# Performance work log

Hardware: AMD Instinct MI355X
Metric: run time of the kernel (lower is better)

The kernel has to match this reference:

```python
import jax, jax.numpy as jnp
import numpy as np

D = 128            # actual_dim / embed_dim
DM = 2 * D         # d_model
HID = 2 * DM       # LSTMCell hidden size
NSYM = 200000
PAD = NSYM
B = 4096
S = 5
NB = 64
STEPS = 4
EPS = 1e-6


def setup_inputs() -> dict:
    key = jax.random.key(0)
    ks = jax.random.split(key, 24)
    def rn(k, sh, scale=0.02):
        return jax.random.normal(k, sh, dtype=jnp.float32) * scale
    emb = rn(ks[10], (NSYM + 1, D)).at[PAD].set(0.0)  # padding row zeroed
    inp = {
        'query': jax.random.randint(ks[0], (B, 2), 0, NSYM),
        'support': jax.random.randint(ks[1], (S, 2), 0, NSYM),
        'q_l_conn': jax.random.randint(ks[2], (B, NB, 2), 0, NSYM),
        'q_l_deg': jax.random.randint(ks[3], (B,), 0, NB),
        'q_r_conn': jax.random.randint(ks[4], (B, NB, 2), 0, NSYM),
        'q_r_deg': jax.random.randint(ks[5], (B,), 0, NB),
        's_l_conn': jax.random.randint(ks[6], (S, NB, 2), 0, NSYM),
        's_l_deg': jax.random.randint(ks[7], (S,), 0, NB),
        's_r_conn': jax.random.randint(ks[8], (S, NB, 2), 0, NSYM),
        's_r_deg': jax.random.randint(ks[9], (S,), 0, NB),
        'emb': emb,
        'gcn_w': rn(ks[11], (D, 2 * D)),
        'gcn_bias': jnp.zeros((D,), jnp.float32),
        'proj1_w': rn(ks[12], (2 * DM, DM)),
        'proj1_b': jnp.zeros((2 * DM,), jnp.float32),
        'proj2_w': rn(ks[13], (DM, 2 * DM)),
        'proj2_b': jnp.zeros((DM,), jnp.float32),
        'ln_g': jnp.ones((DM,), jnp.float32),
        'ln_b': jnp.zeros((DM,), jnp.float32),
        'w_ih': rn(ks[14], (4 * HID, DM)),
        'w_hh': rn(ks[15], (4 * HID, HID)),
        'b_ih': jnp.zeros((4 * HID,), jnp.float32),
        'b_hh': jnp.zeros((4 * HID,), jnp.float32),
    }
    return inp


def _neighbor_encoder(conn, deg, emb, gcn_w, gcn_bias):
    # conn: [N, NB, 2] ids (rel, ent); deg: [N]
    rel = emb[conn[:, :, 0]]                     # [N, NB, D] gather
    ent = emb[conn[:, :, 1]]                     # [N, NB, D] gather
    x = jnp.concatenate([rel, ent], axis=-1)     # [N, NB, 2D]
    out = jnp.einsum('bnd,kd->bnk', x, gcn_w) + gcn_bias  # [N, NB, D]
    denom = jnp.maximum(deg, 1).astype(out.dtype)[:, None]
    return jnp.tanh(out.sum(axis=1) / denom)     # [N, D]


def _support_encoder(x, proj1_w, proj1_b, proj2_w, proj2_b, ln_g, ln_b):
    residual = x
    h = jax.nn.relu(x @ proj1_w.T + proj1_b)
    h = h @ proj2_w.T + proj2_b
    z = h + residual
    mu = z.mean(axis=-1, keepdims=True)
    sigma = jnp.std(z, axis=-1, keepdims=True, ddof=1)
    return ln_g * (z - mu) / (sigma + EPS) + ln_b


def _query_encoder(support_vec, query, w_ih, w_hh, b_ih, b_hh):
    # support_vec: [DM] (single support prototype); query: [B, DM]
    bsz = query.shape[0]
    h_r = jnp.zeros((bsz, HID), query.dtype)
    c = jnp.zeros((bsz, HID), query.dtype)
    xW = query @ w_ih.T + b_ih  # invariant across steps
    h = query
    for _ in range(STEPS):
        gates = xW + h_r @ w_hh.T + b_hh
        i, f, g, o = jnp.split(gates, 4, axis=-1)
        c = jax.nn.sigmoid(f) * c + jax.nn.sigmoid(i) * jnp.tanh(g)
        h_cell = jax.nn.sigmoid(o) * jnp.tanh(c)
        h = query + h_cell[:, :DM]
        # attention over a single support row: softmax of one logit == 1
        r = jnp.broadcast_to(support_vec[None, :], h.shape)
        h_r = jnp.concatenate([h, r], axis=-1)
    return h


def reference(query, support, q_l_conn, q_l_deg, q_r_conn, q_r_deg,
              s_l_conn, s_l_deg, s_r_conn, s_r_deg,
              emb, gcn_w, gcn_bias, proj1_w, proj1_b, proj2_w, proj2_b,
              ln_g, ln_b, w_ih, w_hh, b_ih, b_hh):
    ql = _neighbor_encoder(q_l_conn, q_l_deg, emb, gcn_w, gcn_bias)
    qr = _neighbor_encoder(q_r_conn, q_r_deg, emb, gcn_w, gcn_bias)
    sl = _neighbor_encoder(s_l_conn, s_l_deg, emb, gcn_w, gcn_bias)
    sr = _neighbor_encoder(s_r_conn, s_r_deg, emb, gcn_w, gcn_bias)
    query_nb = jnp.concatenate([ql, qr], axis=-1)    # [B, DM]
    support_nb = jnp.concatenate([sl, sr], axis=-1)  # [S, DM]
    se = lambda x: _support_encoder(x, proj1_w, proj1_b, proj2_w, proj2_b, ln_g, ln_b)
    support_g = se(support_nb).mean(axis=0)          # [DM]
    query_g = se(query_nb)                            # [B, DM]
    query_f = _query_encoder(support_g, query_g, w_ih, w_hh, b_ih, b_hh)
    qn = query_f / jnp.maximum(jnp.linalg.norm(query_f, axis=-1, keepdims=True), 1e-12)
    sn = support_g / jnp.maximum(jnp.linalg.norm(support_g), 1e-12)
    return qn @ sn                                    # [B] matching scores
```

## Files before the change

### kernel.cpp

```cpp
#include <hip/hip_runtime.h>

#define BQ 4096
#define NS 5

typedef __attribute__((ext_vector_type(8))) short bf16x8;
typedef __attribute__((ext_vector_type(4))) float f32x4;
typedef unsigned short ushortT;

#define WS_QNB    0
#define WS_Z      1048576
#define WS_QG     2097152
#define WS_XW     3145728
#define WS_CBUF   5242880
#define WS_XS     6291456
#define WS_H1B    7348224
#define WS_ABF    7872512
#define WS_HB1    8134656
#define WS_P1B    8396800
#define WS_P2B    8462336
#define WS_WIHB   8527872
#define WS_WHHB   8658944
#define WS_GWB    8790016
#define WS_SNB    8806400
#define WS_H1G    8807680
#define WS_ZB     8810240
#define WS_SG     8811520
#define WS_SN     8811776
#define WS_SWL    8812032
#define WS_BL     8813056
#define WS_EMB16  8814080
#define EMB_ELEMS 25600128

__device__ __forceinline__ float wave_allreduce(float v) {
#pragma unroll
  for (int off = 32; off > 0; off >>= 1) v += __shfl_xor(v, off, 64);
  return v;
}
__device__ __forceinline__ float block_allreduce(float v, float* buf) {
  v = wave_allreduce(v);
  __syncthreads();
  if ((threadIdx.x & 63) == 0) buf[threadIdx.x >> 6] = v;
  __syncthreads();
  return buf[0] + buf[1] + buf[2] + buf[3];
}
__device__ __forceinline__ float sigm(float x) { return 1.0f / (1.0f + expf(-x)); }
__device__ __forceinline__ ushortT f2bf(float f) {
  unsigned int u = __float_as_uint(f);
  unsigned int r = (u + 0x7fffu + ((u >> 16) & 1u)) >> 16;
  return (ushortT)r;
}
__device__ __forceinline__ float bf2f(ushortT u) {
  return __uint_as_float(((unsigned int)u) << 16);
}
__device__ __forceinline__ float dot4(float4 a, float4 b) {
  return a.x * b.x + a.y * b.y + a.z * b.z + a.w * b.w;
}

__global__ __launch_bounds__(256) void k_prep(
    const float* __restrict__ emb, ushortT* __restrict__ emb16, int doEmb,
    const float* __restrict__ w_ih, const float* __restrict__ w_hh,
    const float* __restrict__ p1w, const float* __restrict__ p2w,
    const float* __restrict__ gcn_w,
    const float* __restrict__ b_ih, const float* __restrict__ b_hh,
    ushortT* __restrict__ p1b16, ushortT* __restrict__ p2b16,
    ushortT* __restrict__ wihb, ushortT* __restrict__ whhb,
    ushortT* __restrict__ gwb, float* __restrict__ bL) {
  const int gid = blockIdx.x * 256 + threadIdx.x;
  const int stride = gridDim.x * 256;
  if (doEmb) {
    const float4* e4 = (const float4*)emb;
    ushort4* o4 = (ushort4*)emb16;
    for (int i = gid; i < EMB_ELEMS / 4; i += stride) {
      float4 v = e4[i];
      ushort4 u;
      u.x = f2bf(v.x); u.y = f2bf(v.y); u.z = f2bf(v.z); u.w = f2bf(v.w);
      o4[i] = u;
    }
  }
  for (int i = gid; i < 131072; i += stride) p1b16[i] = f2bf(p1w[i]);
  for (int i = gid; i < 131072; i += stride) p2b16[i] = f2bf(p2w[i]);
  for (int i = gid; i < 262144; i += stride) {
    int n = i >> 8, k = i & 255;
    int j = (n >> 2) + 512 * (n & 3);
    wihb[i] = f2bf(w_ih[j * 256 + k]);
    whhb[i] = f2bf(w_hh[j * 512 + k]);
  }
  for (int i = gid; i < 32768; i += stride) gwb[i] = f2bf(gcn_w[i]);
  for (int i = gid; i < 1024; i += stride) {
    int j = (i >> 2) + 512 * (i & 3);
    bL[i] = b_ih[j] + b_hh[j];
  }
}

__global__ __launch_bounds__(256) void k_gather16(
    const int* __restrict__ qlc, const int* __restrict__ qrc,
    const int* __restrict__ slc, const int* __restrict__ src_,
    const ushortT* __restrict__ emb16, ushortT* __restrict__ XS) {
  const int r = blockIdx.x;
  const int b = r >> 1, side = r & 1;
  const int t = threadIdx.x;
  const int* cg;
  if (b < BQ) cg = (side ? qrc : qlc) + (size_t)b * 128;
  else        cg = (side ? src_ : slc) + (size_t)(b - BQ) * 128;
  __shared__ int connS[128];
  __shared__ __align__(16) float part[8][132];
  if (t < 128) connS[t] = cg[t];
  __syncthreads();
  const int s = t >> 5, l = t & 31;
  const ushort4* e2 = (const ushort4*)emb16;
  float4 acc = make_float4(0.f, 0.f, 0.f, 0.f);
  int im[16];
#pragma unroll
  for (int k = 0; k < 16; k++) im[k] = connS[k * 8 + s];
  ushort4 v[16];
#pragma unroll
  for (int k = 0; k < 16; k++) v[k] = e2[(size_t)im[k] * 32 + l];
#pragma unroll
  for (int k = 0; k < 16; k++) {
    acc.x += bf2f(v[k].x); acc.y += bf2f(v[k].y);
    acc.z += bf2f(v[k].z); acc.w += bf2f(v[k].w);
  }
  *(float4*)&part[s][l * 4] = acc;
  __syncthreads();
  const int hf = t >> 7, dd = t & 127;
  float sum = part[hf][dd] + part[2 + hf][dd] + part[4 + hf][dd] + part[6 + hf][dd];
  XS[(size_t)r * 256 + t] = f2bf(sum);
}

__global__ __launch_bounds__(256) void k_gather32(
    const int* __restrict__ qlc, const int* __restrict__ qrc,
    const int* __restrict__ slc, const int* __restrict__ src_,
    const float* __restrict__ emb, ushortT* __restrict__ XS) {
  const int r = blockIdx.x;
  const int b = r >> 1, side = r & 1;
  const int t = threadIdx.x;
  const int* cg;
  if (b < BQ) cg = (side ? qrc : qlc) + (size_t)b * 128;
  else        cg = (side ? src_ : slc) + (size_t)(b - BQ) * 128;
  __shared__ int connS[128];
  __shared__ __align__(16) float part[8][132];
  if (t < 128) connS[t] = cg[t];
  __syncthreads();
  const int s = t >> 5, l = t & 31;
  const float4* emb4 = (const float4*)emb;
  float4 acc = make_float4(0.f, 0.f, 0.f, 0.f);
#pragma unroll
  for (int kb = 0; kb < 2; kb++) {
    int im[8];
#pragma unroll
    for (int k = 0; k < 8; k++) im[k] = connS[(kb * 8 + k) * 8 + s];
    float4 v[8];
#pragma unroll
    for (int k = 0; k < 8; k++) v[k] = emb4[(size_t)im[k] * 32 + l];
#pragma unroll
    for (int k = 0; k < 8; k++) {
      acc.x += v[k].x; acc.y += v[k].y; acc.z += v[k].z; acc.w += v[k].w;
    }
  }
  *(float4*)&part[s][l * 4] = acc;
  __syncthreads();
  const int hf = t >> 7, dd = t & 127;
  float sum = part[hf][dd] + part[2 + hf][dd] + part[4 + hf][dd] + part[6 + hf][dd];
  XS[(size_t)r * 256 + t] = f2bf(sum);
}

__global__ __launch_bounds__(256) void k_gcn(
    const ushortT* __restrict__ XS, const ushortT* __restrict__ gwb,
    const float* __restrict__ gcn_bias,
    const int* __restrict__ qld, const int* __restrict__ qrd,
    const int* __restrict__ sld, const int* __restrict__ srd,
    float* __restrict__ qnb, float* __restrict__ snb, ushortT* __restrict__ xq) {
  __shared__ short As[64 * 40];
  __shared__ short Bs[128 * 40];
  __shared__ int degl[32], degr[32];
  const int t = threadIdx.x;
  const int row0 = blockIdx.x * 64;
  if (t < 32) {
    int b = (row0 >> 1) + t;
    int dl = 1, dr = 1;
    if (b < BQ) { dl = qld[b]; dr = qrd[b]; }
    else if (b < BQ + NS) { dl = sld[b - BQ]; dr = srd[b - BQ]; }
    degl[t] = (dl > 0) ? dl : 1;
    degr[t] = (dr > 0) ? dr : 1;
  }
  const int wave = t >> 6, lane = t & 63;
  const int wm = wave >> 1, wn = wave & 1, quad = lane >> 4, mr = lane & 15;
  f32x4 acc[2][4];
#pragma unroll
  for (int mi = 0; mi < 2; mi++)
#pragma unroll
    for (int ni = 0; ni < 4; ni++) acc[mi][ni] = (f32x4){0.f, 0.f, 0.f, 0.f};
  const int arow = t >> 2, akc = t & 3;
  for (int k0 = 0; k0 < 256; k0 += 32) {
    float4 av = *(const float4*)(XS + (size_t)(row0 + arow) * 256 + k0 + akc * 8);
    float4 bv0 = *(const float4*)(gwb + (size_t)arow * 256 + k0 + akc * 8);
    float4 bv1 = *(const float4*)(gwb + (size_t)(64 + arow) * 256 + k0 + akc * 8);
    __syncthreads();
    *(float4*)&As[arow * 40 + akc * 8] = av;
    *(float4*)&Bs[arow * 40 + akc * 8] = bv0;
    *(float4*)&Bs[(64 + arow) * 40 + akc * 8] = bv1;
    __syncthreads();
    bf16x8 af[2], bfr[4];
#pragma unroll
    for (int mi = 0; mi < 2; mi++)
      af[mi] = *(const bf16x8*)&As[(wm * 32 + mi * 16 + mr) * 40 + quad * 8];
#pragma unroll
    for (int ni = 0; ni < 4; ni++)
      bfr[ni] = *(const bf16x8*)&Bs[(wn * 64 + ni * 16 + mr) * 40 + quad * 8];
#pragma unroll
    for (int mi = 0; mi < 2; mi++)
#pragma unroll
      for (int ni = 0; ni < 4; ni++)
        acc[mi][ni] = __builtin_amdgcn_mfma_f32_16x16x32_bf16(af[mi], bfr[ni], acc[mi][ni], 0, 0, 0);
  }
#pragma unroll
  for (int mi = 0; mi < 2; mi++) {
#pragma unroll
    for (int ni = 0; ni < 4; ni++) {
      const int col = wn * 64 + ni * 16 + mr;
      const int rb = row0 + wm * 32 + mi * 16 + quad * 4;
      const float bs = 64.0f * gcn_bias[col];
#pragma unroll
      for (int reg = 0; reg < 4; reg++) {
        const int row = rb + reg;
        const int b = row >> 1, side = row & 1;
        if (b >= BQ + NS) continue;
        const int li = (row >> 1) - (row0 >> 1);
        const int deg = side ? degr[li] : degl[li];
        float val = tanhf((acc[mi][ni][reg] + bs) / (float)deg);
        if (b < BQ) {
          const size_t o = (size_t)b * 256 + side * 128 + col;
          qnb[o] = val;
          xq[o] = f2bf(val);
        } else {
          snb[(size_t)(b - BQ) * 256 + side * 128 + col] = val;
        }
      }
    }
  }
}

__global__ __launch_bounds__(256) void k_proj1(
    const ushortT* __restrict__ A, const ushortT* __restrict__ B,
    const float* __restrict__ bias, ushortT* __restrict__ outb,
    const float* __restrict__ snb, const float* __restrict__ p1w,
    const float* __restrict__ p1b, float* __restrict__ h1g) {
  __shared__ short As[64 * 40];
  __shared__ short Bs[128 * 40];
  const int t = threadIdx.x;
  if (blockIdx.x >= 256) {
    const int w = (blockIdx.x - 256) * 4 + (t >> 6);
    const int lane = t & 63;
    const int r = w >> 9, j = w & 511;
    float4 x = *(const float4*)&snb[r * 256 + lane * 4];
    float4 wv = *(const float4*)&p1w[(size_t)j * 256 + lane * 4];
    float s = wave_allreduce(dot4(x, wv));
    if (lane == 0) h1g[r * 512 + j] = fmaxf(s + p1b[j], 0.f);
    return;
  }
  const int bn = blockIdx.x % 4, bm = blockIdx.x / 4;
  const int row0 = bm * 64, col0 = bn * 128;
  const int wave = t >> 6, lane = t & 63;
  const int wm = wave >> 1, wn = wave & 1, quad = lane >> 4, mr = lane & 15;
  f32x4 acc[2][4];
#pragma unroll
  for (int mi = 0; mi < 2; mi++)
#pragma unroll
    for (int ni = 0; ni < 4; ni++) acc[mi][ni] = (f32x4){0.f, 0.f, 0.f, 0.f};
  const int arow = t >> 2, akc = t & 3;
  for (int k0 = 0; k0 < 256; k0 += 32) {
    float4 av = *(const float4*)(A + (size_t)(row0 + arow) * 256 + k0 + akc * 8);
    float4 bv0 = *(const float4*)(B + (size_t)(col0 + arow) * 256 + k0 + akc * 8);
    float4 bv1 = *(const float4*)(B + (size_t)(col0 + 64 + arow) * 256 + k0 + akc * 8);
    __syncthreads();
    *(float4*)&As[arow * 40 + akc * 8] = av;
    *(float4*)&Bs[arow * 40 + akc * 8] = bv0;
    *(float4*)&Bs[(64 + arow) * 40 + akc * 8] = bv1;
    __syncthreads();
    bf16x8 af[2], bfr[4];
#pragma unroll
    for (int mi = 0; mi < 2; mi++)
      af[mi] = *(const bf16x8*)&As[(wm * 32 + mi * 16 + mr) * 40 + quad * 8];
#pragma unroll
    for (int ni = 0; ni < 4; ni++)
      bfr[ni] = *(const bf16x8*)&Bs[(wn * 64 + ni * 16 + mr) * 40 + quad * 8];
#pragma unroll
    for (int mi = 0; mi < 2; mi++)
#pragma unroll
      for (int ni = 0; ni < 4; ni++)
        acc[mi][ni] = __builtin_amdgcn_mfma_f32_16x16x32_bf16(af[mi], bfr[ni], acc[mi][ni], 0, 0, 0);
  }
#pragma unroll
  for (int mi = 0; mi < 2; mi++) {
#pragma unroll
    for (int ni = 0; ni < 4; ni++) {
      const int col = col0 + wn * 64 + ni * 16 + mr;
      const int rb = row0 + wm * 32 + mi * 16 + quad * 4;
      const float bs = bias[col];
#pragma unroll
      for (int reg = 0; reg < 4; reg++) {
        const int row = rb + reg;
        outb[(size_t)row * 512 + col] = f2bf(fmaxf(acc[mi][ni][reg] + bs, 0.f));
      }
    }
  }
}

__global__ __launch_bounds__(256) void k_proj2(
    const ushortT* __restrict__ A, const ushortT* __restrict__ B,
    const float* __restrict__ bias, const float* __restrict__ aux,
    float* __restrict__ outf,
    const float* __restrict__ snb, const float* __restrict__ h1g,
    const float* __restrict__ p2w, const float* __restrict__ p2b,
    float* __restrict__ zb) {
  __shared__ short As[64 * 40];
  __shared__ short Bs[128 * 40];
  const int t = threadIdx.x;
  if (blockIdx.x >= 128) {
    const int w = (blockIdx.x - 128) * 4 + (t >> 6);
    const int lane = t & 63;
    const int r = w >> 8, tt = w & 255;
    float4 h0 = *(const float4*)&h1g[r * 512 + lane * 4];
    float4 h1 = *(const float4*)&h1g[r * 512 + 256 + lane * 4];
    float4 w0 = *(const float4*)&p2w[(size_t)tt * 512 + lane * 4];
    float4 w1 = *(const float4*)&p2w[(size_t)tt * 512 + 256 + lane * 4];
    float s = wave_allreduce(dot4(h0, w0) + dot4(h1, w1));
    if (lane == 0) zb[r * 256 + tt] = s + p2b[tt] + snb[r * 256 + tt];
    return;
  }
  const int bn = blockIdx.x % 2, bm = blockIdx.x / 2;
  const int row0 = bm * 64, col0 = bn * 128;
  const int wave = t >> 6, lane = t & 63;
  const int wm = wave >> 1, wn = wave & 1, quad = lane >> 4, mr = lane & 15;
  f32x4 acc[2][4];
#pragma unroll
  for (int mi = 0; mi < 2; mi++)
#pragma unroll
    for (int ni = 0; ni < 4; ni++) acc[mi][ni] = (f32x4){0.f, 0.f, 0.f, 0.f};
  const int arow = t >> 2, akc = t & 3;
  for (int k0 = 0; k0 < 512; k0 += 32) {
    float4 av = *(const float4*)(A + (size_t)(row0 + arow) * 512 + k0 + akc * 8);
    float4 bv0 = *(const float4*)(B + (size_t)(col0 + arow) * 512 + k0 + akc * 8);
    float4 bv1 = *(const float4*)(B + (size_t)(col0 + 64 + arow) * 512 + k0 + akc * 8);
    __syncthreads();
    *(float4*)&As[arow * 40 + akc * 8] = av;
    *(float4*)&Bs[arow * 40 + akc * 8] = bv0;
    *(float4*)&Bs[(64 + arow) * 40 + akc * 8] = bv1;
    __syncthreads();
    bf16x8 af[2], bfr[4];
#pragma unroll
    for (int mi = 0; mi < 2; mi++)
      af[mi] = *(const bf16x8*)&As[(wm * 32 + mi * 16 + mr) * 40 + quad * 8];
#pragma unroll
    for (int ni = 0; ni < 4; ni++)
      bfr[ni] = *(const bf16x8*)&Bs[(wn * 64 + ni * 16 + mr) * 40 + quad * 8];
#pragma unroll
    for (int mi = 0; mi < 2; mi++)
#pragma unroll
      for (int ni = 0; ni < 4; ni++)
        acc[mi][ni] = __builtin_amdgcn_mfma_f32_16x16x32_bf16(af[mi], bfr[ni], acc[mi][ni], 0, 0, 0);
  }
#pragma unroll
  for (int mi = 0; mi < 2; mi++) {
#pragma unroll
    for (int ni = 0; ni < 4; ni++) {
      const int col = col0 + wn * 64 + ni * 16 + mr;
      const int rb = row0 + wm * 32 + mi * 16 + quad * 4;
      const float bs = bias[col];
#pragma unroll
      for (int reg = 0; reg < 4; reg++) {
        const int row = rb + reg;
        const size_t off = (size_t)row * 256 + col;
        outf[off] = acc[mi][ni][reg] + bs + aux[off];
      }
    }
  }
}

__global__ __launch_bounds__(256) void k_ln2(
    const float* __restrict__ Z, const float* __restrict__ ln_g,
    const float* __restrict__ ln_b, float* __restrict__ qg, ushortT* __restrict__ qgb,
    const float* __restrict__ zb, float* __restrict__ sg, float* __restrict__ sn_out) {
  const int t = threadIdx.x;
  if (blockIdx.x >= BQ / 4) {
    __shared__ float rbuf[4];
    float acc = 0.f;
    for (int r = 0; r < NS; r++) {
      float z = zb[r * 256 + t];
      float s = block_allreduce(z, rbuf);
      float mu = s * (1.f / 256.f);
      float dz = z - mu;
      float s2 = block_allreduce(dz * dz, rbuf);
      float rstd = 1.f / (sqrtf(s2 * (1.f / 255.f)) + 1e-6f);
      acc += ln_g[t] * dz * rstd + ln_b[t];
      __syncthreads();
    }
    float g = acc * (1.f / (float)NS);
    sg[t] = g;
    float n2 = block_allreduce(g * g, rbuf);
    sn_out[t] = g / fmaxf(sqrtf(n2), 1e-12f);
    return;
  }
  const int row = blockIdx.x * 4 + (t >> 6);
  const int lane = t & 63;
  float4 z = *(const float4*)&Z[(size_t)row * 256 + lane * 4];
  float s = wave_allreduce(z.x + z.y + z.z + z.w);
  float mu = s * (1.f / 256.f);
  float dx = z.x - mu, dy = z.y - mu, dz = z.z - mu, dw = z.w - mu;
  float s2 = wave_allreduce(dx * dx + dy * dy + dz * dz + dw * dw);
  float rstd = 1.f / (sqrtf(s2 * (1.f / 255.f)) + 1e-6f);
  float4 g = *(const float4*)&ln_g[lane * 4];
  float4 bb = *(const float4*)&ln_b[lane * 4];
  float4 o;
  o.x = g.x * dx * rstd + bb.x;
  o.y = g.y * dy * rstd + bb.y;
  o.z = g.z * dz * rstd + bb.z;
  o.w = g.w * dw * rstd + bb.w;
  *(float4*)&qg[(size_t)row * 256 + lane * 4] = o;
  ushort4 u;
  u.x = f2bf(o.x); u.y = f2bf(o.y); u.z = f2bf(o.z); u.w = f2bf(o.w);
  *(ushort4*)&qgb[(size_t)row * 256 + lane * 4] = u;
}

__global__ __launch_bounds__(256) void k_gemm_lstm(
    const ushortT* __restrict__ A, const ushortT* __restrict__ B,
    const float* __restrict__ bL, float* __restrict__ sWl,
    const float* __restrict__ qg, ushortT* __restrict__ xwb,
    float* __restrict__ cbuf, ushortT* __restrict__ hb_out,
    const float* __restrict__ sg, const float* __restrict__ w_hh, int phase) {
  __shared__ short As[64 * 40];
  __shared__ short Bs[128 * 40];
  __shared__ __align__(16) float Cs[64 * 132];
  const int t = threadIdx.x;
  if (blockIdx.x >= 512) {
    const int n = (blockIdx.x - 512) * 4 + (t >> 6);
    const int lane = t & 63;
    const int j = (n >> 2) + 512 * (n & 3);
    float4 x = *(const float4*)&sg[lane * 4];
    float4 wv = *(const float4*)&w_hh[(size_t)j * 512 + 256 + lane * 4];
    float s = wave_allreduce(dot4(x, wv));
    if (lane == 0) sWl[n] = s;
    return;
  }
  const int bn = blockIdx.x & 7, bm = blockIdx.x >> 3;
  const int row0 = bm * 64, col0 = bn * 128;
  const int wave = t >> 6, lane = t & 63;
  const int wm = wave >> 1, wn = wave & 1, quad = lane >> 4, mr = lane & 15;
  f32x4 acc[2][4];
#pragma unroll
  for (int mi = 0; mi < 2; mi++)
#pragma unroll
    for (int ni = 0; ni < 4; ni++) acc[mi][ni] = (f32x4){0.f, 0.f, 0.f, 0.f};
  const int arow = t >> 2, akc = t & 3;
  for (int k0 = 0; k0 < 256; k0 += 32) {
    float4 av = *(const float4*)(A + (size_t)(row0 + arow) * 256 + k0 + akc * 8);
    float4 bv0 = *(const float4*)(B + (size_t)(col0 + arow) * 256 + k0 + akc * 8);
    float4 bv1 = *(const float4*)(B + (size_t)(col0 + 64 + arow) * 256 + k0 + akc * 8);
    __syncthreads();
    *(float4*)&As[arow * 40 + akc * 8] = av;
    *(float4*)&Bs[arow * 40 + akc * 8] = bv0;
    *(float4*)&Bs[(64 + arow) * 40 + akc * 8] = bv1;
    __syncthreads();
    bf16x8 af[2], bfr[4];
#pragma unroll
    for (int mi = 0; mi < 2; mi++)
      af[mi] = *(const bf16x8*)&As[(wm * 32 + mi * 16 + mr) * 40 + quad * 8];
#pragma unroll
    for (int ni = 0; ni < 4; ni++)
      bfr[ni] = *(const bf16x8*)&Bs[(wn * 64 + ni * 16 + mr) * 40 + quad * 8];
#pragma unroll
    for (int mi = 0; mi < 2; mi++)
#pragma unroll
      for (int ni = 0; ni < 4; ni++)
        acc[mi][ni] = __builtin_amdgcn_mfma_f32_16x16x32_bf16(af[mi], bfr[ni], acc[mi][ni], 0, 0, 0);
  }
#pragma unroll
  for (int mi = 0; mi < 2; mi++)
#pragma unroll
    for (int ni = 0; ni < 4; ni++)
#pragma unroll
      for (int reg = 0; reg < 4; reg++)
        Cs[(wm * 32 + mi * 16 + quad * 4 + reg) * 132 + wn * 64 + ni * 16 + mr] =
            acc[mi][ni][reg];
  __syncthreads();
  const int u = t & 31, grp = t >> 5;
  const int ugl = bn * 32 + u;
#pragma unroll
  for (int i = 0; i < 8; i++) {
    const int rl = grp * 8 + i;
    const int row = row0 + rl;
    const size_t o = (size_t)row * 256 + ugl;
    float4 gv = *(const float4*)&Cs[rl * 132 + u * 4];
    if (phase == 0) {
      float4 bb = *(const float4*)&bL[col0 + u * 4];
      gv.x += bb.x; gv.y += bb.y; gv.z += bb.z; gv.w += bb.w;
      float c0 = sigm(gv.x) * tanhf(gv.z);
      float h = qg[o] + sigm(gv.w) * tanhf(c0);
      cbuf[o] = c0;
      hb_out[o] = f2bf(h);
      ushort4 xo;
      xo.x = f2bf(gv.x); xo.y = f2bf(gv.y);
      xo.z = f2bf(gv.z); xo.w = f2bf(gv.w);
      *(ushort4*)&xwb[(size_t)row * 1024 + col0 + u * 4] = xo;
    } else {
      ushort4 xv = *(const ushort4*)&xwb[(size_t)row * 1024 + col0 + u * 4];
      float4 sv = *(const float4*)&sWl[col0 + u * 4];
      gv.x += bf2f(xv.x) + sv.x; gv.y += bf2f(xv.y) + sv.y;
      gv.z += bf2f(xv.z) + sv.z; gv.w += bf2f(xv.w) + sv.w;
      float c = sigm(gv.y) * cbuf[o] + sigm(gv.x) * tanhf(gv.z);
      float h = qg[o] + sigm(gv.w) * tanhf(c);
      if (phase == 2) {
        cbuf[o] = h;
      } else {
        cbuf[o] = c;
        hb_out[o] = f2bf(h);
      }
    }
  }
}

__global__ __launch_bounds__(256) void k_out(
    const float* __restrict__ hf, const float* __restrict__ sn, float* __restrict__ out) {
  const int t = threadIdx.x;
  const int row = blockIdx.x * 4 + (t >> 6);
  const int lane = t & 63;
  float4 h = *(const float4*)&hf[(size_t)row * 256 + lane * 4];
  float4 s = *(const float4*)&sn[lane * 4];
  float dt = wave_allreduce(dot4(h, s));
  float nr = wave_allreduce(dot4(h, h));
  if (lane == 0) out[row] = dt / fmaxf(sqrtf(nr), 1e-12f);
}

extern "C" void kernel_launch(void* const* d_in, const int* in_sizes, int n_in,
                              void* d_out, int out_size, void* d_ws, size_t ws_size,
                              hipStream_t stream) {
  const int* q_l_conn = (const int*)d_in[2];
  const int* q_l_deg  = (const int*)d_in[3];
  const int* q_r_conn = (const int*)d_in[4];
  const int* q_r_deg  = (const int*)d_in[5];
  const int* s_l_conn = (const int*)d_in[6];
  const int* s_l_deg  = (const int*)d_in[7];
  const int* s_r_conn = (const int*)d_in[8];
  const int* s_r_deg  = (const int*)d_in[9];
  const float* emb      = (const float*)d_in[10];
  const float* gcn_w    = (const float*)d_in[11];
  const float* gcn_bias = (const float*)d_in[12];
  const float* proj1_w  = (const float*)d_in[13];
  const float* proj1_b  = (const float*)d_in[14];
  const float* proj2_w  = (const float*)d_in[15];
  const float* proj2_b  = (const float*)d_in[16];
  const float* ln_g     = (const float*)d_in[17];
  const float* ln_b     = (const float*)d_in[18];
  const float* w_ih     = (const float*)d_in[19];
  const float* w_hh     = (const float*)d_in[20];
  const float* b_ih     = (const float*)d_in[21];
  const float* b_hh     = (const float*)d_in[22];

  float* ws = (float*)d_ws;
  float* qnb   = ws + WS_QNB;
  float* Z     = ws + WS_Z;
  float* qg    = ws + WS_QG;
  ushortT* xwb = (ushortT*)(ws + WS_XW);
  float* cbuf  = ws + WS_CBUF;
  ushortT* XS    = (ushortT*)(ws + WS_XS);
  ushortT* h1b   = (ushortT*)(ws + WS_H1B);
  ushortT* abf   = (ushortT*)(ws + WS_ABF);
  ushortT* hb1   = (ushortT*)(ws + WS_HB1);
  ushortT* p1b16 = (ushortT*)(ws + WS_P1B);
  ushortT* p2b16 = (ushortT*)(ws + WS_P2B);
  ushortT* wihb  = (ushortT*)(ws + WS_WIHB);
  ushortT* whhb  = (ushortT*)(ws + WS_WHHB);
  ushortT* gwb   = (ushortT*)(ws + WS_GWB);
  float* snb   = ws + WS_SNB;
  float* h1g   = ws + WS_H1G;
  float* zb    = ws + WS_ZB;
  float* sg    = ws + WS_SG;
  float* sn    = ws + WS_SN;
  float* sWl   = ws + WS_SWL;
  float* bL    = ws + WS_BL;
  ushortT* emb16 = (ushortT*)(ws + WS_EMB16);
  float* out   = (float*)d_out;

  const size_t needF = (size_t)WS_EMB16 + (EMB_ELEMS + 1) / 2;
  const int useBf16 = (ws_size >= needF * sizeof(float)) ? 1 : 0;

  hipLaunchKernelGGL(k_prep, dim3(2048), dim3(256), 0, stream,
                     emb, emb16, useBf16,
                     w_ih, w_hh, proj1_w, proj2_w, gcn_w, b_ih, b_hh,
                     p1b16, p2b16, wihb, whhb, gwb, bL);
  if (useBf16) {
    hipLaunchKernelGGL(k_gather16, dim3(2 * (BQ + NS)), dim3(256), 0, stream,
                       q_l_conn, q_r_conn, s_l_conn, s_r_conn, emb16, XS);
  } else {
    hipLaunchKernelGGL(k_gather32, dim3(2 * (BQ + NS)), dim3(256), 0, stream,
                       q_l_conn, q_r_conn, s_l_conn, s_r_conn, emb, XS);
  }
  hipLaunchKernelGGL(k_gcn, dim3(129), dim3(256), 0, stream,
                     XS, gwb, gcn_bias, q_l_deg, q_r_deg, s_l_deg, s_r_deg,
                     qnb, snb, abf);
  hipLaunchKernelGGL(k_proj1, dim3(256 + 640), dim3(256), 0, stream,
                     abf, p1b16, proj1_b, h1b,
                     snb, proj1_w, proj1_b, h1g);
  hipLaunchKernelGGL(k_proj2, dim3(128 + 320), dim3(256), 0, stream,
                     h1b, p2b16, proj2_b, qnb, Z,
                     snb, h1g, proj2_w, proj2_b, zb);
  hipLaunchKernelGGL(k_ln2, dim3(BQ / 4 + 1), dim3(256), 0, stream,
                     Z, ln_g, ln_b, qg, abf, zb, sg, sn);
  hipLaunchKernelGGL(k_gemm_lstm, dim3(512 + 256), dim3(256), 0, stream,
                     abf, wihb, bL, sWl, qg, xwb, cbuf, hb1, sg, w_hh, 0);
  hipLaunchKernelGGL(k_gemm_lstm, dim3(512), dim3(256), 0, stream,
                     hb1, whhb, bL, sWl, qg, xwb, cbuf, abf, sg, w_hh, 1);
  hipLaunchKernelGGL(k_gemm_lstm, dim3(512), dim3(256), 0, stream,
                     abf, whhb, bL, sWl, qg, xwb, cbuf, hb1, sg, w_hh, 1);
  hipLaunchKernelGGL(k_gemm_lstm, dim3(512), dim3(256), 0, stream,
                     hb1, whhb, bL, sWl, qg, xwb, cbuf, (ushortT*)nullptr, sg, w_hh, 2);
  hipLaunchKernelGGL(k_out, dim3(BQ / 4), dim3(256), 0, stream, cbuf, sn, out);
}
```

Measured before the change: 333.1 us.

## Fuse all four LSTM steps and the output dot into one row-strip kernel

Replaces the four separate LSTM GEMM launches and the output kernel with a single kernel in which each block owns 16 query rows and runs every step, keeping h, c and the query state in shared memory. The constant support half of the hidden input is now folded into the GEMM as a K=512 bf16 weight (with a bf16 copy of support_g) instead of a separate fp32 matvec. This removes the global round-trips of xw, c and h between steps and several launches. In exchange it launches only 256 blocks, each streaming the whole weight matrix from global/L2 without LDS staging, and adds K work for the support part.

```diff
diff --git a/kernel.cpp b/kernel.cpp
--- a/kernel.cpp
+++ b/kernel.cpp
@@ -10,7 +10,7 @@
 #define WS_QNB    0
 #define WS_Z      1048576
 #define WS_QG     2097152
-#define WS_XW     3145728
+#define WS_WHH2   3145728
 #define WS_CBUF   5242880
 #define WS_XS     6291456
 #define WS_H1B    7348224
@@ -26,7 +26,7 @@
 #define WS_ZB     8810240
 #define WS_SG     8811520
 #define WS_SN     8811776
-#define WS_SWL    8812032
+#define WS_SGB    8812032
 #define WS_BL     8813056
 #define WS_EMB16  8814080
 #define EMB_ELEMS 25600128
@@ -63,7 +63,7 @@
     const float* __restrict__ gcn_w,
     const float* __restrict__ b_ih, const float* __restrict__ b_hh,
     ushortT* __restrict__ p1b16, ushortT* __restrict__ p2b16,
-    ushortT* __restrict__ wihb, ushortT* __restrict__ whhb,
+    ushortT* __restrict__ wihb, ushortT* __restrict__ whh2,
     ushortT* __restrict__ gwb, float* __restrict__ bL) {
   const int gid = blockIdx.x * 256 + threadIdx.x;
   const int stride = gridDim.x * 256;
@@ -83,7 +83,11 @@
     int n = i >> 8, k = i & 255;
     int j = (n >> 2) + 512 * (n & 3);
     wihb[i] = f2bf(w_ih[j * 256 + k]);
-    whhb[i] = f2bf(w_hh[j * 512 + k]);
+  }
+  for (int i = gid; i < 524288; i += stride) {
+    int n = i >> 9, k = i & 511;
+    int j = (n >> 2) + 512 * (n & 3);
+    whh2[i] = f2bf(w_hh[j * 512 + k]);
   }
   for (int i = gid; i < 32768; i += stride) gwb[i] = f2bf(gcn_w[i]);
   for (int i = gid; i < 1024; i += stride) {
@@ -99,12 +103,12 @@
   const int r = blockIdx.x;
   const int b = r >> 1, side = r & 1;
   const int t = threadIdx.x;
-  const int* cg;
-  if (b < BQ) cg = (side ? qrc : qlc) + (size_t)b * 128;
-  else        cg = (side ? src_ : slc) + (size_t)(b - BQ) * 128;
+  const int* cg2;
+  if (b < BQ) cg2 = (side ? qrc : qlc) + (size_t)b * 128;
+  else        cg2 = (side ? src_ : slc) + (size_t)(b - BQ) * 128;
   __shared__ int connS[128];
   __shared__ __align__(16) float part[8][132];
-  if (t < 128) connS[t] = cg[t];
+  if (t < 128) connS[t] = cg2[t];
   __syncthreads();
   const int s = t >> 5, l = t & 31;
   const ushort4* e2 = (const ushort4*)emb16;
@@ -134,12 +138,12 @@
   const int r = blockIdx.x;
   const int b = r >> 1, side = r & 1;
   const int t = threadIdx.x;
-  const int* cg;
-  if (b < BQ) cg = (side ? qrc : qlc) + (size_t)b * 128;
-  else        cg = (side ? src_ : slc) + (size_t)(b - BQ) * 128;
+  const int* cg2;
+  if (b < BQ) cg2 = (side ? qrc : qlc) + (size_t)b * 128;
+  else        cg2 = (side ? src_ : slc) + (size_t)(b - BQ) * 128;
   __shared__ int connS[128];
   __shared__ __align__(16) float part[8][132];
-  if (t < 128) connS[t] = cg[t];
+  if (t < 128) connS[t] = cg2[t];
   __syncthreads();
   const int s = t >> 5, l = t & 31;
   const float4* emb4 = (const float4*)emb;
@@ -380,7 +384,8 @@
 __global__ __launch_bounds__(256) void k_ln2(
     const float* __restrict__ Z, const float* __restrict__ ln_g,
     const float* __restrict__ ln_b, float* __restrict__ qg, ushortT* __restrict__ qgb,
-    const float* __restrict__ zb, float* __restrict__ sg, float* __restrict__ sn_out) {
+    const float* __restrict__ zb, float* __restrict__ sg, float* __restrict__ sn_out,
+    ushortT* __restrict__ sgb) {
   const int t = threadIdx.x;
   if (blockIdx.x >= BQ / 4) {
     __shared__ float rbuf[4];
@@ -397,6 +402,7 @@
     }
     float g = acc * (1.f / (float)NS);
     sg[t] = g;
+    sgb[t] = f2bf(g);
     float n2 = block_allreduce(g * g, rbuf);
     sn_out[t] = g / fmaxf(sqrtf(n2), 1e-12f);
     return;
@@ -422,113 +428,100 @@
   *(ushort4*)&qgb[(size_t)row * 256 + lane * 4] = u;
 }
 
-__global__ __launch_bounds__(256) void k_gemm_lstm(
-    const ushortT* __restrict__ A, const ushortT* __restrict__ B,
-    const float* __restrict__ bL, float* __restrict__ sWl,
-    const float* __restrict__ qg, ushortT* __restrict__ xwb,
-    float* __restrict__ cbuf, ushortT* __restrict__ hb_out,
-    const float* __restrict__ sg, const float* __restrict__ w_hh, int phase) {
-  __shared__ short As[64 * 40];
-  __shared__ short Bs[128 * 40];
-  __shared__ __align__(16) float Cs[64 * 132];
+__global__ __launch_bounds__(256) void k_lstm_strip(
+    const ushortT* __restrict__ qgb, const float* __restrict__ qg,
+    const ushortT* __restrict__ wihb, const ushortT* __restrict__ whh2,
+    const float* __restrict__ bL, const ushortT* __restrict__ sgb,
+    const float* __restrict__ sn, float* __restrict__ out) {
+  __shared__ __align__(16) ushortT hS[16][264];
+  __shared__ __align__(16) float qgS[16][256];
+  __shared__ __align__(16) float cS[16][256];
+  __shared__ __align__(16) float hF[16][256];
+  __shared__ __align__(16) ushortT sgS[264];
   const int t = threadIdx.x;
-  if (blockIdx.x >= 512) {
-    const int n = (blockIdx.x - 512) * 4 + (t >> 6);
-    const int lane = t & 63;
-    const int j = (n >> 2) + 512 * (n & 3);
-    float4 x = *(const float4*)&sg[lane * 4];
-    float4 wv = *(const float4*)&w_hh[(size_t)j * 512 + 256 + lane * 4];
-    float s = wave_allreduce(dot4(x, wv));
-    if (lane == 0) sWl[n] = s;
-    return;
-  }
-  const int bn = blockIdx.x & 7, bm = blockIdx.x >> 3;
-  const int row0 = bm * 64, col0 = bn * 128;
-  const int wave = t >> 6, lane = t & 63;
-  const int wm = wave >> 1, wn = wave & 1, quad = lane >> 4, mr = lane & 15;
-  f32x4 acc[2][4];
-#pragma unroll
-  for (int mi = 0; mi < 2; mi++)
-#pragma unroll
-    for (int ni = 0; ni < 4; ni++) acc[mi][ni] = (f32x4){0.f, 0.f, 0.f, 0.f};
-  const int arow = t >> 2, akc = t & 3;
-  for (int k0 = 0; k0 < 256; k0 += 32) {
-    float4 av = *(const float4*)(A + (size_t)(row0 + arow) * 256 + k0 + akc * 8);
-    float4 bv0 = *(const float4*)(B + (size_t)(col0 + arow) * 256 + k0 + akc * 8);
-    float4 bv1 = *(const float4*)(B + (size_t)(col0 + 64 + arow) * 256 + k0 + akc * 8);
-    __syncthreads();
-    *(float4*)&As[arow * 40 + akc * 8] = av;
-    *(float4*)&Bs[arow * 40 + akc * 8] = bv0;
-    *(float4*)&Bs[(64 + arow) * 40 + akc * 8] = bv1;
-    __syncthreads();
-    bf16x8 af[2], bfr[4];
-#pragma unroll
-    for (int mi = 0; mi < 2; mi++)
-      af[mi] = *(const bf16x8*)&As[(wm * 32 + mi * 16 + mr) * 40 + quad * 8];
-#pragma unroll
-    for (int ni = 0; ni < 4; ni++)
-      bfr[ni] = *(const bf16x8*)&Bs[(wn * 64 + ni * 16 + mr) * 40 + quad * 8];
-#pragma unroll
-    for (int mi = 0; mi < 2; mi++)
-#pragma unroll
-      for (int ni = 0; ni < 4; ni++)
-        acc[mi][ni] = __builtin_amdgcn_mfma_f32_16x16x32_bf16(af[mi], bfr[ni], acc[mi][ni], 0, 0, 0);
-  }
-#pragma unroll
-  for (int mi = 0; mi < 2; mi++)
-#pragma unroll
-    for (int ni = 0; ni < 4; ni++)
-#pragma unroll
-      for (int reg = 0; reg < 4; reg++)
-        Cs[(wm * 32 + mi * 16 + quad * 4 + reg) * 132 + wn * 64 + ni * 16 + mr] =
-            acc[mi][ni][reg];
+  const int w = t >> 6, lane = t & 63;
+  const int quad = lane >> 4, mr = lane & 15;
+  const int r0 = blockIdx.x * 16;
+  const int n0 = w * 256;
+  for (int i = t; i < 16 * 256; i += 256) {
+    int r = i >> 8, c = i & 255;
+    qgS[r][c] = qg[(size_t)(r0 + r) * 256 + c];
+  }
+  sgS[t] = sgb[t];
   __syncthreads();
-  const int u = t & 31, grp = t >> 5;
-  const int ugl = bn * 32 + u;
-#pragma unroll
-  for (int i = 0; i < 8; i++) {
-    const int rl = grp * 8 + i;
-    const int row = row0 + rl;
-    const size_t o = (size_t)row * 256 + ugl;
-    float4 gv = *(const float4*)&Cs[rl * 132 + u * 4];
-    if (phase == 0) {
-      float4 bb = *(const float4*)&bL[col0 + u * 4];
-      gv.x += bb.x; gv.y += bb.y; gv.z += bb.z; gv.w += bb.w;
-      float c0 = sigm(gv.x) * tanhf(gv.z);
-      float h = qg[o] + sigm(gv.w) * tanhf(c0);
-      cbuf[o] = c0;
-      hb_out[o] = f2bf(h);
-      ushort4 xo;
-      xo.x = f2bf(gv.x); xo.y = f2bf(gv.y);
-      xo.z = f2bf(gv.z); xo.w = f2bf(gv.w);
-      *(ushort4*)&xwb[(size_t)row * 1024 + col0 + u * 4] = xo;
-    } else {
-      ushort4 xv = *(const ushort4*)&xwb[(size_t)row * 1024 + col0 + u * 4];
-      float4 sv = *(const float4*)&sWl[col0 + u * 4];
-      gv.x += bf2f(xv.x) + sv.x; gv.y += bf2f(xv.y) + sv.y;
-      gv.z += bf2f(xv.z) + sv.z; gv.w += bf2f(xv.w) + sv.w;
-      float c = sigm(gv.y) * cbuf[o] + sigm(gv.x) * tanhf(gv.z);
-      float h = qg[o] + sigm(gv.w) * tanhf(c);
-      if (phase == 2) {
-        cbuf[o] = h;
+  float bLs[16];
+#pragma unroll
+  for (int ct = 0; ct < 16; ct++) bLs[ct] = bL[n0 + ct * 16 + mr];
+
+  f32x4 accv[16];
+  f32x4 xwv[16];
+  const int base = lane & ~3;
+
+#pragma unroll
+  for (int p = 0; p < 4; p++) {
+    const int K = (p == 0) ? 256 : 512;
+    const ushortT* Bp = (p == 0) ? wihb : whh2;
+#pragma unroll
+    for (int ct = 0; ct < 16; ct++) accv[ct] = (f32x4){0.f, 0.f, 0.f, 0.f};
+    for (int k0 = 0; k0 < K; k0 += 32) {
+      bf16x8 af;
+      if (p == 0)
+        af = *(const bf16x8*)&qgb[(size_t)(r0 + mr) * 256 + k0 + quad * 8];
+      else if (k0 < 256)
+        af = *(const bf16x8*)&hS[mr][k0 + quad * 8];
+      else
+        af = *(const bf16x8*)&sgS[(k0 - 256) + quad * 8];
+#pragma unroll
+      for (int ct = 0; ct < 16; ct++) {
+        bf16x8 bf = *(const bf16x8*)&Bp[(size_t)(n0 + ct * 16 + mr) * K + k0 + quad * 8];
+        accv[ct] = __builtin_amdgcn_mfma_f32_16x16x32_bf16(af, bf, accv[ct], 0, 0, 0);
+      }
+    }
+    __syncthreads();
+#pragma unroll
+    for (int ct = 0; ct < 16; ct++) {
+      if (p == 0) {
+        accv[ct][0] += bLs[ct]; accv[ct][1] += bLs[ct];
+        accv[ct][2] += bLs[ct]; accv[ct][3] += bLs[ct];
+        xwv[ct] = accv[ct];
       } else {
-        cbuf[o] = c;
-        hb_out[o] = f2bf(h);
+        accv[ct][0] += xwv[ct][0]; accv[ct][1] += xwv[ct][1];
+        accv[ct][2] += xwv[ct][2]; accv[ct][3] += xwv[ct][3];
       }
-    }
-  }
-}
-
-__global__ __launch_bounds__(256) void k_out(
-    const float* __restrict__ hf, const float* __restrict__ sn, float* __restrict__ out) {
-  const int t = threadIdx.x;
-  const int row = blockIdx.x * 4 + (t >> 6);
-  const int lane = t & 63;
-  float4 h = *(const float4*)&hf[(size_t)row * 256 + lane * 4];
-  float4 s = *(const float4*)&sn[lane * 4];
-  float dt = wave_allreduce(dot4(h, s));
-  float nr = wave_allreduce(dot4(h, h));
-  if (lane == 0) out[row] = dt / fmaxf(sqrtf(nr), 1e-12f);
+      f32x4 gi = accv[ct];
+      f32x4 gf, gg, go;
+#pragma unroll
+      for (int c = 0; c < 4; c++) {
+        gf[c] = __shfl(gi[c], base + 1, 64);
+        gg[c] = __shfl(gi[c], base + 2, 64);
+        go[c] = __shfl(gi[c], base + 3, 64);
+      }
+      if ((lane & 3) == 0) {
+        const int u = (n0 + ct * 16 + mr) >> 2;
+#pragma unroll
+        for (int reg = 0; reg < 4; reg++) {
+          const int r = quad * 4 + reg;
+          float c_;
+          if (p == 0) c_ = sigm(gi[reg]) * tanhf(gg[reg]);
+          else        c_ = sigm(gf[reg]) * cS[r][u] + sigm(gi[reg]) * tanhf(gg[reg]);
+          float h = qgS[r][u] + sigm(go[reg]) * tanhf(c_);
+          cS[r][u] = c_;
+          if (p < 3) hS[r][u] = f2bf(h);
+          else       hF[r][u] = h;
+        }
+      }
+    }
+    __syncthreads();
+  }
+  float4 snv = *(const float4*)&sn[lane * 4];
+#pragma unroll
+  for (int rr = 0; rr < 4; rr++) {
+    const int r = w * 4 + rr;
+    float4 h = *(const float4*)&hF[r][lane * 4];
+    float dt = wave_allreduce(dot4(h, snv));
+    float nr = wave_allreduce(dot4(h, h));
+    if (lane == 0) out[r0 + r] = dt / fmaxf(sqrtf(nr), 1e-12f);
+  }
 }
 
 extern "C" void kernel_launch(void* const* d_in, const int* in_sizes, int n_in,
@@ -560,23 +553,20 @@
   float* qnb   = ws + WS_QNB;
   float* Z     = ws + WS_Z;
   float* qg    = ws + WS_QG;
-  ushortT* xwb = (ushortT*)(ws + WS_XW);
-  float* cbuf  = ws + WS_CBUF;
+  ushortT* whh2  = (ushortT*)(ws + WS_WHH2);
   ushortT* XS    = (ushortT*)(ws + WS_XS);
   ushortT* h1b   = (ushortT*)(ws + WS_H1B);
   ushortT* abf   = (ushortT*)(ws + WS_ABF);
-  ushortT* hb1   = (ushortT*)(ws + WS_HB1);
   ushortT* p1b16 = (ushortT*)(ws + WS_P1B);
   ushortT* p2b16 = (ushortT*)(ws + WS_P2B);
   ushortT* wihb  = (ushortT*)(ws + WS_WIHB);
-  ushortT* whhb  = (ushortT*)(ws + WS_WHHB);
   ushortT* gwb   = (ushortT*)(ws + WS_GWB);
   float* snb   = ws + WS_SNB;
   float* h1g   = ws + WS_H1G;
   float* zb    = ws + WS_ZB;
   float* sg    = ws + WS_SG;
   float* sn    = ws + WS_SN;
-  float* sWl   = ws + WS_SWL;
+  ushortT* sgb = (ushortT*)(ws + WS_SGB);
   float* bL    = ws + WS_BL;
   ushortT* emb16 = (ushortT*)(ws + WS_EMB16);
   float* out   = (float*)d_out;
@@ -587,7 +577,7 @@
   hipLaunchKernelGGL(k_prep, dim3(2048), dim3(256), 0, stream,
                      emb, emb16, useBf16,
                      w_ih, w_hh, proj1_w, proj2_w, gcn_w, b_ih, b_hh,
-                     p1b16, p2b16, wihb, whhb, gwb, bL);
+                     p1b16, p2b16, wihb, whh2, gwb, bL);
   if (useBf16) {
     hipLaunchKernelGGL(k_gather16, dim3(2 * (BQ + NS)), dim3(256), 0, stream,
                        q_l_conn, q_r_conn, s_l_conn, s_r_conn, emb16, XS);
@@ -605,14 +595,7 @@
                      h1b, p2b16, proj2_b, qnb, Z,
                      snb, h1g, proj2_w, proj2_b, zb);
   hipLaunchKernelGGL(k_ln2, dim3(BQ / 4 + 1), dim3(256), 0, stream,
-                     Z, ln_g, ln_b, qg, abf, zb, sg, sn);
-  hipLaunchKernelGGL(k_gemm_lstm, dim3(512 + 256), dim3(256), 0, stream,
-                     abf, wihb, bL, sWl, qg, xwb, cbuf, hb1, sg, w_hh, 0);
-  hipLaunchKernelGGL(k_gemm_lstm, dim3(512), dim3(256), 0, stream,
-                     hb1, whhb, bL, sWl, qg, xwb, cbuf, abf, sg, w_hh, 1);
-  hipLaunchKernelGGL(k_gemm_lstm, dim3(512), dim3(256), 0, stream,
-                     abf, whhb, bL, sWl, qg, xwb, cbuf, hb1, sg, w_hh, 1);
-  hipLaunchKernelGGL(k_gemm_lstm, dim3(512), dim3(256), 0, stream,
-                     hb1, whhb, bL, sWl, qg, xwb, cbuf, (ushortT*)nullptr, sg, w_hh, 2);
-  hipLaunchKernelGGL(k_out, dim3(BQ / 4), dim3(256), 0, stream, cbuf, sn, out);
-}
+                     Z, ln_g, ln_b, qg, abf, zb, sg, sn, sgb);
+  hipLaunchKernelGGL(k_lstm_strip, dim3(256), dim3(256), 0, stream,
+                     abf, qg, wihb, whh2, bL, sgb, sn, out);
+}
```

Measured after the change: 537.2 us. 1.61x slower.
